# Performance work log

Hardware: AMD Instinct MI355X
Metric: run time of the kernel (lower is better)

The kernel has to match this reference:

```python
import jax, jax.numpy as jnp
import numpy as np

NORM = 20.0   # from dataset 'NETS'
ALPHA = 1.0
EPS = 1e-12   # torch F.normalize eps


def _l2_normalize(x):
    n = jnp.sqrt(jnp.sum(x * x, axis=-1, keepdims=True))
    return x / jnp.maximum(n, EPS)


def setup_inputs() -> dict:
    key = jax.random.key(0)
    k1, k2, k3, k4, k5 = jax.random.split(key, 5)
    B, P, C = 4096, 32, 512
    predicted_score = jax.random.uniform(k1, (B,), dtype=jnp.float32) * NORM
    targets = jax.random.uniform(k2, (B,), dtype=jnp.float32) * NORM
    feats = jax.random.normal(k3, (B, C), dtype=jnp.float32)
    pivot_features = jax.random.normal(k4, (B, P, C), dtype=jnp.float32)
    pivot_scores = jax.random.uniform(k5, (B, P), dtype=jnp.float32) * NORM
    return {
        "predicted_score": predicted_score,
        "targets": targets,
        "feats": feats,
        "pivot_features": pivot_features,
        "pivot_scores": pivot_scores,
    }


def reference(predicted_score, targets, feats, pivot_features, pivot_scores):
    scale = ALPHA * NORM
    f = _l2_normalize(feats)                      # (B, C)
    pf = _l2_normalize(pivot_features)            # (B, P, C)
    ps = pivot_scores.astype(jnp.float32)         # (B, P)

    # image-text: (B,1,C) @ (B,C,P) -> (B,P)
    it_matches = jnp.einsum('bc,bpc->bp', f, pf)
    it_label = 1.0 - 2.0 * jnp.abs(targets[:, None] - ps) / scale
    image_text_loss = jnp.mean(jnp.abs(it_matches - it_label))

    # image-image: (B,B)
    ii_matches = f @ f.T
    ii_label = 1.0 - 2.0 * jnp.abs(targets[:, None] - targets[None, :]) / scale
    image_image_loss = jnp.mean(jnp.abs(ii_matches - ii_label))

    # text-text: (B,P,P)
    tt_matches = jnp.einsum('bpc,bqc->bpq', pf, pf)
    tt_label = 1.0 - 2.0 * jnp.abs(ps[:, :, None] - ps[:, None, :]) / scale
    text_text_loss = jnp.mean(jnp.abs(tt_matches - tt_label))

    mae_loss = jnp.mean(jnp.abs(predicted_score - targets))

    return (image_image_loss, text_text_loss, image_text_loss, mae_loss)
```

## Files before the change

kernel.cpp:

```cpp
#include <hip/hip_runtime.h>
#include <hip/hip_bf16.h>
#include <stdint.h>

#define B_N 4096
#define P_N 32
#define C_N 512
#define LABC 0.1f
#define N_II 528
#define GRID_TOTAL (N_II * 9)

typedef float  floatx4 __attribute__((ext_vector_type(4)));
typedef __bf16 bf16x8  __attribute__((ext_vector_type(8)));

__device__ __forceinline__ unsigned short f2bf(float x) {
    return __builtin_bit_cast(unsigned short, __float2bfloat16(x));
}
__device__ __forceinline__ uint4 pack8(const float4& v0, const float4& v1) {
    uint4 pk;
    pk.x = (unsigned)f2bf(v0.x) | ((unsigned)f2bf(v0.y) << 16);
    pk.y = (unsigned)f2bf(v0.z) | ((unsigned)f2bf(v0.w) << 16);
    pk.z = (unsigned)f2bf(v1.x) | ((unsigned)f2bf(v1.y) << 16);
    pk.w = (unsigned)f2bf(v1.z) | ((unsigned)f2bf(v1.w) << 16);
    return pk;
}
__device__ __forceinline__ void bfly_reduce2(float& a, float& b) {
#pragma unroll
    for (int m = 1; m < 64; m <<= 1) {
        a += __shfl_xor(a, m, 64);
        b += __shfl_xor(b, m, 64);
    }
}
__device__ __forceinline__ void bfly_reduce1(float& a) {
#pragma unroll
    for (int m = 1; m < 64; m <<= 1) a += __shfl_xor(a, m, 64);
}

#define ACC_II 0
#define ACC_TT 8
#define ACC_IT 16

__global__ __launch_bounds__(256) void k_prep(const float* __restrict__ feats,
                                              const float* __restrict__ pred,
                                              const float* __restrict__ targ,
                                              unsigned short* __restrict__ fb,
                                              double* __restrict__ acc,
                                              float* __restrict__ maePart) {
    const int wave = threadIdx.x >> 6, lane = threadIdx.x & 63;
    const int row = blockIdx.x * 4 + wave;
    const float* src = feats + (size_t)row * C_N + lane * 8;
    float4 v0 = *(const float4*)src;
    float4 v1 = *(const float4*)(src + 4);
    float ss = v0.x*v0.x + v0.y*v0.y + v0.z*v0.z + v0.w*v0.w
             + v1.x*v1.x + v1.y*v1.y + v1.z*v1.z + v1.w*v1.w;
    bfly_reduce1(ss);
    const float inv = rsqrtf(fmaxf(ss, 1e-24f));
    float4 n0 = {v0.x*inv, v0.y*inv, v0.z*inv, v0.w*inv};
    float4 n1 = {v1.x*inv, v1.y*inv, v1.z*inv, v1.w*inv};
    *(uint4*)(fb + (size_t)row * C_N + lane * 8) = pack8(n0, n1);

    if (wave == 0) {
        float v = 0.f;
        if (lane < 4) {
            const int r = blockIdx.x * 4 + lane;
            v = fabsf(pred[r] - targ[r]);
        }
        v += __shfl_xor(v, 1, 64);
        v += __shfl_xor(v, 2, 64);
        if (lane == 0) maePart[blockIdx.x] = v;
    }
    if (blockIdx.x == 0 && threadIdx.x < 24) acc[threadIdx.x] = 0.0;
}

#define APAD 130
struct TTsm {
    unsigned short pfs[64 * 33 * 8];
    float psS[P_N];
    float rdiag[P_N];
    float redT[4], redI[4];
};
struct IIsm {
    unsigned short As[4 * APAD * 8];
    unsigned short Bs[4 * APAD * 8];
    float tm[128], tn[128];
    float red[4];
};
union SMu { TTsm tt; IIsm ii; };

__global__ __launch_bounds__(256) void k_fused(const float* __restrict__ pf_g,
                                               const float* __restrict__ ps_g,
                                               const float* __restrict__ targets,
                                               const unsigned short* __restrict__ fb,
                                               double* __restrict__ acc) {
    __shared__ __align__(16) SMu sm;
    const int tid = threadIdx.x, wave = tid >> 6, lane = tid & 63;
    const int quad = lane >> 4, l15 = lane & 15;
    const int bid = blockIdx.x;
    const bool isII = (bid % 9) == 0;

    if (isII) {
        IIsm& S = sm.ii;
        int bm = 0, rem = bid / 9;
        while (rem >= 32 - bm) { rem -= 32 - bm; ++bm; }
        const int bn = bm + rem;
        const int wr = wave >> 1, wc = wave & 1;
        const int mbase = bm * 128, nbase = bn * 128;

        if (tid < 128) S.tm[tid] = targets[mbase + tid];
        else           S.tn[tid - 128] = targets[nbase + tid - 128];

        const int row = tid >> 1, half = tid & 1;
        const unsigned short* aSrc = fb + (size_t)(mbase + row) * C_N + half * 16;
        const unsigned short* bSrc = fb + (size_t)(nbase + row) * C_N + half * 16;
        const int c0 = half * 2, c1 = half * 2 + 1;

        floatx4 accv[16];
#pragma unroll
        for (int i = 0; i < 16; ++i) accv[i] = (floatx4){0.f, 0.f, 0.f, 0.f};

        uint4 a0 = *(const uint4*)(aSrc);
        uint4 a1 = *(const uint4*)(aSrc + 8);
        uint4 b0 = *(const uint4*)(bSrc);
        uint4 b1 = *(const uint4*)(bSrc + 8);

        for (int ks = 0; ks < 16; ++ks) {
            __syncthreads();
            *(uint4*)&S.As[((size_t)c0 * APAD + row) * 8] = a0;
            *(uint4*)&S.As[((size_t)c1 * APAD + row) * 8] = a1;
            *(uint4*)&S.Bs[((size_t)c0 * APAD + row) * 8] = b0;
            *(uint4*)&S.Bs[((size_t)c1 * APAD + row) * 8] = b1;
            __syncthreads();
            if (ks < 15) {
                const int off = (ks + 1) * 32;
                a0 = *(const uint4*)(aSrc + off);
                a1 = *(const uint4*)(aSrc + off + 8);
                b0 = *(const uint4*)(bSrc + off);
                b1 = *(const uint4*)(bSrc + off + 8);
            }
            bf16x8 af[4], bfv[4];
#pragma unroll
            for (int t = 0; t < 4; ++t)
                af[t] = __builtin_bit_cast(bf16x8, *(const uint4*)&S.As[((size_t)quad * APAD + wr * 64 + t * 16 + l15) * 8]);
#pragma unroll
            for (int t = 0; t < 4; ++t)
                bfv[t] = __builtin_bit_cast(bf16x8, *(const uint4*)&S.Bs[((size_t)quad * APAD + wc * 64 + t * 16 + l15) * 8]);
#pragma unroll
            for (int ti = 0; ti < 4; ++ti)
#pragma unroll
                for (int tj = 0; tj < 4; ++tj)
                    accv[ti * 4 + tj] = __builtin_amdgcn_mfma_f32_16x16x32_bf16(af[ti], bfv[tj], accv[ti * 4 + tj], 0, 0, 0);
        }

        float s = 0.f;
#pragma unroll
        for (int ti = 0; ti < 4; ++ti)
#pragma unroll
            for (int tj = 0; tj < 4; ++tj)
#pragma unroll
                for (int r = 0; r < 4; ++r) {
                    const int p = wr * 64 + ti * 16 + quad * 4 + r;
                    const int q = wc * 64 + tj * 16 + l15;
                    const float lab = 1.f - LABC * fabsf(S.tm[p] - S.tn[q]);
                    s += fabsf(accv[ti * 4 + tj][r] - lab);
                }
        if (bm != bn) s *= 2.f;
        bfly_reduce1(s);
        if (lane == 0) S.red[wave] = s;
        __syncthreads();
        if (tid == 0) atomicAdd(&acc[ACC_II], (double)(S.red[0] + S.red[1] + S.red[2] + S.red[3]));
    } else {
        const int b = bid - (bid / 9) - 1;
        if (b >= B_N) return;
        TTsm& S = sm.tt;

        if (tid < P_N) S.psS[tid] = ps_g[b * P_N + tid];
        const float tb = targets[b];

        const float* base = pf_g + (size_t)b * P_N * C_N;
#pragma unroll
        for (int i = 0; i < 8; ++i) {
            const int r = wave * 8 + i;
            const float* src = base + r * C_N + lane * 8;
            float4 v0 = *(const float4*)src;
            float4 v1 = *(const float4*)(src + 4);
            *(uint4*)&S.pfs[((size_t)lane * 33 + r) * 8] = pack8(v0, v1);
        }
        if (wave == 0) {
            uint4 f = *(const uint4*)(fb + (size_t)b * C_N + lane * 8);
            *(uint4*)&S.pfs[((size_t)lane * 33 + 32) * 8] = f;
        }
        __syncthreads();

        const int pt = (wave >> 1) * 16, qt = (wave & 1) * 16;
        const bool doF = (wave < 2);
        floatx4 acc4 = {0.f, 0.f, 0.f, 0.f};
        floatx4 accF = {0.f, 0.f, 0.f, 0.f};
        const uint4 zero4 = {0u, 0u, 0u, 0u};
#pragma unroll
        for (int kk = 0; kk < 16; ++kk) {
            const int ch = kk * 4 + quad;
            bf16x8 a = __builtin_bit_cast(bf16x8, *(const uint4*)&S.pfs[((size_t)ch * 33 + pt + l15) * 8]);
            bf16x8 bb = __builtin_bit_cast(bf16x8, *(const uint4*)&S.pfs[((size_t)ch * 33 + qt + l15) * 8]);
            acc4 = __builtin_amdgcn_mfma_f32_16x16x32_bf16(a, bb, acc4, 0, 0, 0);
            if (doF) {
                uint4 fr = *(const uint4*)&S.pfs[((size_t)ch * 33 + 32) * 8];
                bf16x8 af = __builtin_bit_cast(bf16x8, (l15 == 0) ? fr : zero4);
                accF = __builtin_amdgcn_mfma_f32_16x16x32_bf16(af, bb, accF, 0, 0, 0);
            }
        }
        if (pt == qt) {
            if ((l15 >> 2) == quad) S.rdiag[pt + l15] = rsqrtf(fmaxf(acc4[l15 & 3], 1e-24f));
        }
        __syncthreads();

        float tt_sum = 0.f, it_sum = 0.f;
#pragma unroll
        for (int r = 0; r < 4; ++r) {
            const int p = pt + quad * 4 + r;
            const int q = qt + l15;
            const float val = acc4[r] * S.rdiag[p] * S.rdiag[q];
            const float lab = 1.f - LABC * fabsf(S.psS[p] - S.psS[q]);
            tt_sum += fabsf(val - lab);
        }
        if (doF && quad == 0) {
            const int q = qt + l15;
            const float val = accF[0] * S.rdiag[q];
            const float lab = 1.f - LABC * fabsf(tb - S.psS[q]);
            it_sum = fabsf(val - lab);
        }
        bfly_reduce2(tt_sum, it_sum);
        if (lane == 0) { S.redT[wave] = tt_sum; S.redI[wave] = it_sum; }
        __syncthreads();
        if (tid == 0) {
            atomicAdd(&acc[ACC_TT], (double)(S.redT[0] + S.redT[1] + S.redT[2] + S.redT[3]));
            atomicAdd(&acc[ACC_IT], (double)(S.redI[0] + S.redI[1] + S.redI[2] + S.redI[3]));
        }
    }
}

__global__ __launch_bounds__(256) void k_final(const double* __restrict__ acc,
                                               const float* __restrict__ maePart,
                                               float* __restrict__ out) {
    __shared__ float red[4];
    const int tid = threadIdx.x, wave = tid >> 6, lane = tid & 63;
    float s = maePart[tid] + maePart[tid + 256] + maePart[tid + 512] + maePart[tid + 768];
    bfly_reduce1(s);
    if (lane == 0) red[wave] = s;
    __syncthreads();
    if (tid == 0) {
        out[0] = (float)(acc[ACC_II] / (double)((size_t)B_N * B_N));
        out[1] = (float)(acc[ACC_TT] / (double)((size_t)B_N * P_N * P_N));
        out[2] = (float)(acc[ACC_IT] / (double)((size_t)B_N * P_N));
        out[3] = (red[0] + red[1] + red[2] + red[3]) * (1.f / B_N);
    }
}

extern "C" void kernel_launch(void* const* d_in, const int* in_sizes, int n_in,
                              void* d_out, int out_size, void* d_ws, size_t ws_size,
                              hipStream_t stream) {
    const float* pred  = (const float*)d_in[0];
    const float* targ  = (const float*)d_in[1];
    const float* feats = (const float*)d_in[2];
    const float* pf    = (const float*)d_in[3];
    const float* ps    = (const float*)d_in[4];
    float* out = (float*)d_out;

    double* acc         = (double*)d_ws;
    float* maePart      = (float*)((char*)d_ws + 256);
    unsigned short* fb  = (unsigned short*)((char*)d_ws + 8192);

    k_prep<<<B_N / 4, 256, 0, stream>>>(feats, pred, targ, fb, acc, maePart);
    k_fused<<<GRID_TOTAL, 256, 0, stream>>>(pf, ps, targ, fb, acc);
    k_final<<<1, 256, 0, stream>>>(acc, maePart, out);
}
```

Baseline: 379.8 us.

## Replace global double atomics with per-block partials and batch pivot loads into registers

Each block now writes its partial sums to per-block slots in workspace, and the final kernel reduces them, replacing contended double-precision atomicAdds on three global accumulators. The text-text path also issues all of its global loads for pivot features and the normalized feature row into registers before converting and storing to LDS, so more memory requests are in flight at once. This raises register pressure (16 uint4 per thread) and adds a larger reduction in the single-block final kernel.

```diff
diff --git a/kernel.cpp b/kernel.cpp
--- a/kernel.cpp
+++ b/kernel.cpp
@@ -8,6 +8,7 @@
 #define LABC 0.1f
 #define N_II 528
 #define GRID_TOTAL (N_II * 9)
+#define N_TT (GRID_TOTAL - N_II)
 
 typedef float  floatx4 __attribute__((ext_vector_type(4)));
 typedef __bf16 bf16x8  __attribute__((ext_vector_type(8)));
@@ -35,15 +36,10 @@
     for (int m = 1; m < 64; m <<= 1) a += __shfl_xor(a, m, 64);
 }
 
-#define ACC_II 0
-#define ACC_TT 8
-#define ACC_IT 16
-
 __global__ __launch_bounds__(256) void k_prep(const float* __restrict__ feats,
                                               const float* __restrict__ pred,
                                               const float* __restrict__ targ,
                                               unsigned short* __restrict__ fb,
-                                              double* __restrict__ acc,
                                               float* __restrict__ maePart) {
     const int wave = threadIdx.x >> 6, lane = threadIdx.x & 63;
     const int row = blockIdx.x * 4 + wave;
@@ -68,7 +64,6 @@
         v += __shfl_xor(v, 2, 64);
         if (lane == 0) maePart[blockIdx.x] = v;
     }
-    if (blockIdx.x == 0 && threadIdx.x < 24) acc[threadIdx.x] = 0.0;
 }
 
 #define APAD 130
@@ -90,7 +85,9 @@
                                                const float* __restrict__ ps_g,
                                                const float* __restrict__ targets,
                                                const unsigned short* __restrict__ fb,
-                                               double* __restrict__ acc) {
+                                               double* __restrict__ partII,
+                                               double* __restrict__ partTT,
+                                               double* __restrict__ partIT) {
     __shared__ __align__(16) SMu sm;
     const int tid = threadIdx.x, wave = tid >> 6, lane = tid & 63;
     const int quad = lane >> 4, l15 = lane & 15;
@@ -166,28 +163,36 @@
         bfly_reduce1(s);
         if (lane == 0) S.red[wave] = s;
         __syncthreads();
-        if (tid == 0) atomicAdd(&acc[ACC_II], (double)(S.red[0] + S.red[1] + S.red[2] + S.red[3]));
+        if (tid == 0) partII[bid / 9] = (double)(S.red[0] + S.red[1] + S.red[2] + S.red[3]);
     } else {
         const int b = bid - (bid / 9) - 1;
-        if (b >= B_N) return;
         TTsm& S = sm.tt;
-
+        if (b >= B_N) {
+            if (tid == 0) { partTT[b] = 0.0; partIT[b] = 0.0; }
+            return;
+        }
+
+        const float* base = pf_g + (size_t)b * P_N * C_N;
+        uint4 st[16];
+#pragma unroll
+        for (int i = 0; i < 8; ++i) {
+            const float* src = base + (wave * 8 + i) * C_N + lane * 8;
+            st[2 * i]     = *(const uint4*)src;
+            st[2 * i + 1] = *(const uint4*)(src + 4);
+        }
+        uint4 fReg = {0u, 0u, 0u, 0u};
+        if (wave == 0) fReg = *(const uint4*)(fb + (size_t)b * C_N + lane * 8);
         if (tid < P_N) S.psS[tid] = ps_g[b * P_N + tid];
         const float tb = targets[b];
 
-        const float* base = pf_g + (size_t)b * P_N * C_N;
 #pragma unroll
         for (int i = 0; i < 8; ++i) {
             const int r = wave * 8 + i;
-            const float* src = base + r * C_N + lane * 8;
-            float4 v0 = *(const float4*)src;
-            float4 v1 = *(const float4*)(src + 4);
+            const float4 v0 = __builtin_bit_cast(float4, st[2 * i]);
+            const float4 v1 = __builtin_bit_cast(float4, st[2 * i + 1]);
             *(uint4*)&S.pfs[((size_t)lane * 33 + r) * 8] = pack8(v0, v1);
         }
-        if (wave == 0) {
-            uint4 f = *(const uint4*)(fb + (size_t)b * C_N + lane * 8);
-            *(uint4*)&S.pfs[((size_t)lane * 33 + 32) * 8] = f;
-        }
+        if (wave == 0) *(uint4*)&S.pfs[((size_t)lane * 33 + 32) * 8] = fReg;
         __syncthreads();
 
         const int pt = (wave >> 1) * 16, qt = (wave & 1) * 16;
@@ -231,26 +236,43 @@
         if (lane == 0) { S.redT[wave] = tt_sum; S.redI[wave] = it_sum; }
         __syncthreads();
         if (tid == 0) {
-            atomicAdd(&acc[ACC_TT], (double)(S.redT[0] + S.redT[1] + S.redT[2] + S.redT[3]));
-            atomicAdd(&acc[ACC_IT], (double)(S.redI[0] + S.redI[1] + S.redI[2] + S.redI[3]));
-        }
-    }
-}
-
-__global__ __launch_bounds__(256) void k_final(const double* __restrict__ acc,
+            partTT[b] = (double)(S.redT[0] + S.redT[1] + S.redT[2] + S.redT[3]);
+            partIT[b] = (double)(S.redI[0] + S.redI[1] + S.redI[2] + S.redI[3]);
+        }
+    }
+}
+
+__global__ __launch_bounds__(256) void k_final(const double* __restrict__ partII,
+                                               const double* __restrict__ partTT,
+                                               const double* __restrict__ partIT,
                                                const float* __restrict__ maePart,
                                                float* __restrict__ out) {
-    __shared__ float red[4];
+    __shared__ double redA[4], redB[4], redC[4];
+    __shared__ float redM[4];
     const int tid = threadIdx.x, wave = tid >> 6, lane = tid & 63;
-    float s = maePart[tid] + maePart[tid + 256] + maePart[tid + 512] + maePart[tid + 768];
-    bfly_reduce1(s);
-    if (lane == 0) red[wave] = s;
+
+    double sII = 0.0, sTT = 0.0, sIT = 0.0;
+    for (int i = tid; i < N_II; i += 256) sII += partII[i];
+    for (int i = tid; i < N_TT; i += 256) { sTT += partTT[i]; sIT += partIT[i]; }
+    float sM = maePart[tid] + maePart[tid + 256] + maePart[tid + 512] + maePart[tid + 768];
+
+#pragma unroll
+    for (int m = 1; m < 64; m <<= 1) {
+        sII += __shfl_xor(sII, m, 64);
+        sTT += __shfl_xor(sTT, m, 64);
+        sIT += __shfl_xor(sIT, m, 64);
+        sM  += __shfl_xor(sM, m, 64);
+    }
+    if (lane == 0) { redA[wave] = sII; redB[wave] = sTT; redC[wave] = sIT; redM[wave] = sM; }
     __syncthreads();
     if (tid == 0) {
-        out[0] = (float)(acc[ACC_II] / (double)((size_t)B_N * B_N));
-        out[1] = (float)(acc[ACC_TT] / (double)((size_t)B_N * P_N * P_N));
-        out[2] = (float)(acc[ACC_IT] / (double)((size_t)B_N * P_N));
-        out[3] = (red[0] + red[1] + red[2] + red[3]) * (1.f / B_N);
+        const double ii = redA[0] + redA[1] + redA[2] + redA[3];
+        const double tt = redB[0] + redB[1] + redB[2] + redB[3];
+        const double it = redC[0] + redC[1] + redC[2] + redC[3];
+        out[0] = (float)(ii / (double)((size_t)B_N * B_N));
+        out[1] = (float)(tt / (double)((size_t)B_N * P_N * P_N));
+        out[2] = (float)(it / (double)((size_t)B_N * P_N));
+        out[3] = (redM[0] + redM[1] + redM[2] + redM[3]) * (1.f / B_N);
     }
 }
 
@@ -264,11 +286,13 @@
     const float* ps    = (const float*)d_in[4];
     float* out = (float*)d_out;
 
-    double* acc         = (double*)d_ws;
-    float* maePart      = (float*)((char*)d_ws + 256);
-    unsigned short* fb  = (unsigned short*)((char*)d_ws + 8192);
-
-    k_prep<<<B_N / 4, 256, 0, stream>>>(feats, pred, targ, fb, acc, maePart);
-    k_fused<<<GRID_TOTAL, 256, 0, stream>>>(pf, ps, targ, fb, acc);
-    k_final<<<1, 256, 0, stream>>>(acc, maePart, out);
-}
+    float* maePart      = (float*)d_ws;
+    double* partII      = (double*)((char*)d_ws + 4096);
+    double* partTT      = (double*)((char*)d_ws + 16384);
+    double* partIT      = (double*)((char*)d_ws + 65536);
+    unsigned short* fb  = (unsigned short*)((char*)d_ws + 131072);
+
+    k_prep<<<B_N / 4, 256, 0, stream>>>(feats, pred, targ, fb, maePart);
+    k_fused<<<GRID_TOTAL, 256, 0, stream>>>(pf, ps, targ, fb, partII, partTT, partIT);
+    k_final<<<1, 256, 0, stream>>>(partII, partTT, partIT, maePart, out);
+}
```

After: 382.6 us. About the same (+0.7%).
